# Kernel optimization log

Measured on AMD Instinct MI355X. Metric: run time of the kernel, lower is better.

## Reference

```python
import jax, jax.numpy as jnp
import numpy as np

N_NODES = 100000
N_EDGES = 1600000
DIM = 32
BN_EPS = 1e-5


def setup_inputs() -> dict:
    key = jax.random.key(0)
    ks = jax.random.split(key, 5)
    h = jax.random.normal(ks[0], (N_NODES, DIM), dtype=jnp.float32)
    e = jax.random.normal(ks[1], (N_EDGES, DIM), dtype=jnp.float32)
    norm = jax.random.uniform(ks[2], (N_NODES, 1), dtype=jnp.float32)
    src = jax.random.randint(ks[3], (N_EDGES,), 0, N_NODES, dtype=jnp.int32)
    dst = jax.random.randint(ks[4], (N_EDGES,), 0, N_NODES, dtype=jnp.int32)
    return {
        "h": h, "e": e, "norm": norm, "src": src, "dst": dst,
        "gamma_h": jnp.ones((DIM,), jnp.float32),
        "beta_h": jnp.zeros((DIM,), jnp.float32),
        "gamma_e": jnp.ones((DIM,), jnp.float32),
        "beta_e": jnp.zeros((DIM,), jnp.float32),
    }


def _batch_norm(x, gamma, beta):
    # training-mode BatchNorm1d: biased batch statistics over axis 0
    mean = jnp.mean(x, axis=0)
    var = jnp.var(x, axis=0)
    return (x - mean) * jax.lax.rsqrt(var + BN_EPS) * gamma + beta


def reference(h, e, norm, src, dst, gamma_h, beta_h, gamma_e, beta_e):
    n_nodes = h.shape[0]
    h = h * norm                                  # [N, d]
    # per-edge gate: e_ij = Ce + Dh_src + Eh_dst (all identity projections)
    e_ij = e + h[src] + h[dst]                    # [E, d]
    sigma = jax.nn.sigmoid(e_ij)                  # [E, d]
    # gated weighted-mean aggregation onto destination nodes
    num = jax.ops.segment_sum(sigma * h[src], dst, num_segments=n_nodes)
    den = jax.ops.segment_sum(sigma, dst, num_segments=n_nodes)
    h_new = h + num / (den + 1e-6)                # zero-indegree nodes: h + 0
    h_new = h_new * norm
    # batch norm (training mode), then activation; dropout is identity in eval
    h_out = jax.nn.relu(_batch_norm(h_new, gamma_h, beta_h))
    e_out = jax.nn.relu(_batch_norm(e_ij, gamma_e, beta_e))
    return h_out, e_out
```

## Files before the change

kernel.cpp:

```cpp
#include <hip/hip_runtime.h>

#define NN 100000
#define NE 1600000
#define DIMS 32
static constexpr int SCOPIES = 32;

typedef float fx4 __attribute__((ext_vector_type(4)));

#define SCAN_NB  128
#define SCAN_NTH 256
#define SCAN_CPT 4

static constexpr long long OFF_HNB  = 0;
static constexpr long long OFF_DEG  = 1600000;
static constexpr long long OFF_SE   = 1700000;
static constexpr long long OFF_SH   = 1702048;
static constexpr long long OFF_FIN  = 1704096;
static constexpr long long OFF_OFFS = 1704224;
static constexpr long long OFF_CURS = 1804232;
static constexpr long long OFF_TEX  = 1904232;
static constexpr long long OFF_PART = 1937000;
static constexpr long long OFF_EID2 = 1937128;

__device__ __forceinline__ ushort bf16rn(float f) {
  unsigned u = __float_as_uint(f);
  unsigned r = (u + 0x7FFFu + ((u >> 16) & 1u)) >> 16;
  return (ushort)r;
}
__device__ __forceinline__ float bf16tof(ushort s) {
  return __uint_as_float(((unsigned)s) << 16);
}

__global__ __launch_bounds__(256) void k_hn(const float* __restrict__ h,
                                            const float* __restrict__ norm,
                                            ushort* __restrict__ hnb) {
  int i = blockIdx.x * blockDim.x + threadIdx.x;
  if (i >= NN * 8) return;
  float4 v = reinterpret_cast<const float4*>(h)[i];
  float nm = norm[i >> 3];
  ushort4 o;
  o.x = bf16rn(v.x * nm);
  o.y = bf16rn(v.y * nm);
  o.z = bf16rn(v.z * nm);
  o.w = bf16rn(v.w * nm);
  reinterpret_cast<ushort4*>(hnb)[i] = o;
}

__global__ __launch_bounds__(256) void k_hist(const int* __restrict__ dst,
                                              int* __restrict__ deg) {
  int i = blockIdx.x * blockDim.x + threadIdx.x;
  if (i >= NE / 4) return;
  int4 d = reinterpret_cast<const int4*>(dst)[i];
  atomicAdd(&deg[d.x], 1);
  atomicAdd(&deg[d.y], 1);
  atomicAdd(&deg[d.z], 1);
  atomicAdd(&deg[d.w], 1);
}

__global__ __launch_bounds__(SCAN_NTH) void k_scanA(const int* __restrict__ deg,
                                                    int* __restrict__ texcl,
                                                    int* __restrict__ partials) {
  const int t = threadIdx.x, b = blockIdx.x;
  const int tid = b * SCAN_NTH + t;
  const int lo = tid * SCAN_CPT;
  const int hi = (lo + SCAN_CPT < NN) ? lo + SCAN_CPT : NN;
  int s = 0;
  for (int i = lo; i < hi; ++i) s += deg[i];
  __shared__ int sh[SCAN_NTH];
  sh[t] = s;
  __syncthreads();
  for (int d = 1; d < SCAN_NTH; d <<= 1) {
    int v = (t >= d) ? sh[t - d] : 0;
    __syncthreads();
    sh[t] += v;
    __syncthreads();
  }
  texcl[b * SCAN_NTH + t] = sh[t] - s;
  if (t == SCAN_NTH - 1) partials[b] = sh[t];
}

__global__ __launch_bounds__(SCAN_NB) void k_scanB(int* __restrict__ partials) {
  __shared__ int sh[SCAN_NB];
  const int t = threadIdx.x;
  int v = partials[t];
  sh[t] = v;
  __syncthreads();
  for (int d = 1; d < SCAN_NB; d <<= 1) {
    int u = (t >= d) ? sh[t - d] : 0;
    __syncthreads();
    sh[t] += u;
    __syncthreads();
  }
  partials[t] = sh[t] - v;
}

__global__ __launch_bounds__(SCAN_NTH) void k_scanC(const int* __restrict__ deg,
                                                    const int* __restrict__ texcl,
                                                    const int* __restrict__ partials,
                                                    int* __restrict__ offs,
                                                    int* __restrict__ curs) {
  const int t = threadIdx.x, b = blockIdx.x;
  const int tid = b * SCAN_NTH + t;
  const int lo = tid * SCAN_CPT;
  const int hi = (lo + SCAN_CPT < NN) ? lo + SCAN_CPT : NN;
  int run = partials[b] + texcl[b * SCAN_NTH + t];
  for (int i = lo; i < hi; ++i) {
    offs[i] = run;
    curs[i] = run;
    run += deg[i];
  }
  if (tid == 0) offs[NN] = NE;
}

__global__ __launch_bounds__(256) void k_edge(const float* __restrict__ e,
                                              const ushort* __restrict__ hnb,
                                              const int* __restrict__ src,
                                              const int* __restrict__ dst,
                                              int* __restrict__ curs,
                                              int2* __restrict__ eid2,
                                              float* __restrict__ stats_e) {
  const int lane = threadIdx.x & 7;
  const int slot0 = (blockIdx.x * blockDim.x + threadIdx.x) >> 3;
  const int S = (gridDim.x * blockDim.x) >> 3;
  float s0 = 0.f, s1 = 0.f, s2 = 0.f, s3 = 0.f;
  float q0 = 0.f, q1 = 0.f, q2 = 0.f, q3 = 0.f;

  const float4*  e4  = reinterpret_cast<const float4*>(e);
  const ushort4* hb4 = reinterpret_cast<const ushort4*>(hnb);

  for (int base = slot0; base < NE; base += 4 * S) {
    const int k0 = base;
    const int k1 = base + S;
    const int k2 = base + 2 * S;
    const int k3 = base + 3 * S;
    const bool v1 = (k1 < NE), v2 = (k2 < NE), v3 = (k3 < NE);
    const int a1 = v1 ? k1 : k0, a2 = v2 ? k2 : k0, a3 = v3 ? k3 : k0;
    const int sc0 = src[k0], dc0 = dst[k0];
    const int sc1 = src[a1], dc1 = dst[a1];
    const int sc2 = src[a2], dc2 = dst[a2];
    const int sc3 = src[a3], dc3 = dst[a3];
    float4  ev0 = e4[(long long)k0 * 8 + lane];
    float4  ev1 = e4[(long long)a1 * 8 + lane];
    float4  ev2 = e4[(long long)a2 * 8 + lane];
    float4  ev3 = e4[(long long)a3 * 8 + lane];
    ushort4 hs0 = hb4[(long long)sc0 * 8 + lane];
    ushort4 hs1 = hb4[(long long)sc1 * 8 + lane];
    ushort4 hs2 = hb4[(long long)sc2 * 8 + lane];
    ushort4 hs3 = hb4[(long long)sc3 * 8 + lane];
    ushort4 hd0 = hb4[(long long)dc0 * 8 + lane];
    ushort4 hd1 = hb4[(long long)dc1 * 8 + lane];
    ushort4 hd2 = hb4[(long long)dc2 * 8 + lane];
    ushort4 hd3 = hb4[(long long)dc3 * 8 + lane];
    if (lane == 0) {
      { int pos = atomicAdd(&curs[dc0], 1); eid2[pos] = make_int2(k0, sc0); }
      if (v1) { int pos = atomicAdd(&curs[dc1], 1); eid2[pos] = make_int2(k1, sc1); }
      if (v2) { int pos = atomicAdd(&curs[dc2], 1); eid2[pos] = make_int2(k2, sc2); }
      if (v3) { int pos = atomicAdd(&curs[dc3], 1); eid2[pos] = make_int2(k3, sc3); }
    }
    {
      float x0 = ev0.x + bf16tof(hs0.x) + bf16tof(hd0.x);
      float x1 = ev0.y + bf16tof(hs0.y) + bf16tof(hd0.y);
      float x2 = ev0.z + bf16tof(hs0.z) + bf16tof(hd0.z);
      float x3 = ev0.w + bf16tof(hs0.w) + bf16tof(hd0.w);
      s0 += x0; s1 += x1; s2 += x2; s3 += x3;
      q0 += x0 * x0; q1 += x1 * x1; q2 += x2 * x2; q3 += x3 * x3;
    }
    if (v1) {
      float x0 = ev1.x + bf16tof(hs1.x) + bf16tof(hd1.x);
      float x1 = ev1.y + bf16tof(hs1.y) + bf16tof(hd1.y);
      float x2 = ev1.z + bf16tof(hs1.z) + bf16tof(hd1.z);
      float x3 = ev1.w + bf16tof(hs1.w) + bf16tof(hd1.w);
      s0 += x0; s1 += x1; s2 += x2; s3 += x3;
      q0 += x0 * x0; q1 += x1 * x1; q2 += x2 * x2; q3 += x3 * x3;
    }
    if (v2) {
      float x0 = ev2.x + bf16tof(hs2.x) + bf16tof(hd2.x);
      float x1 = ev2.y + bf16tof(hs2.y) + bf16tof(hd2.y);
      float x2 = ev2.z + bf16tof(hs2.z) + bf16tof(hd2.z);
      float x3 = ev2.w + bf16tof(hs2.w) + bf16tof(hd2.w);
      s0 += x0; s1 += x1; s2 += x2; s3 += x3;
      q0 += x0 * x0; q1 += x1 * x1; q2 += x2 * x2; q3 += x3 * x3;
    }
    if (v3) {
      float x0 = ev3.x + bf16tof(hs3.x) + bf16tof(hd3.x);
      float x1 = ev3.y + bf16tof(hs3.y) + bf16tof(hd3.y);
      float x2 = ev3.z + bf16tof(hs3.z) + bf16tof(hd3.z);
      float x3 = ev3.w + bf16tof(hs3.w) + bf16tof(hd3.w);
      s0 += x0; s1 += x1; s2 += x2; s3 += x3;
      q0 += x0 * x0; q1 += x1 * x1; q2 += x2 * x2; q3 += x3 * x3;
    }
  }

  __shared__ float sh[64];
  if (threadIdx.x < 64) sh[threadIdx.x] = 0.f;
  __syncthreads();
  const int cb = lane * 4;
  atomicAdd(&sh[cb + 0], s0); atomicAdd(&sh[cb + 1], s1);
  atomicAdd(&sh[cb + 2], s2); atomicAdd(&sh[cb + 3], s3);
  atomicAdd(&sh[32 + cb + 0], q0); atomicAdd(&sh[32 + cb + 1], q1);
  atomicAdd(&sh[32 + cb + 2], q2); atomicAdd(&sh[32 + cb + 3], q3);
  __syncthreads();
  if (threadIdx.x < 64)
    atomicAdd(&stats_e[(blockIdx.x & (SCOPIES - 1)) * 64 + threadIdx.x], sh[threadIdx.x]);
}

__global__ void k_fin_e(const float* __restrict__ stats_e, float* __restrict__ fin) {
  int t = threadIdx.x;
  float s = 0.f, q = 0.f;
  for (int c = 0; c < SCOPIES; ++c) {
    s += stats_e[c * 64 + t];
    q += stats_e[c * 64 + 32 + t];
  }
  float mean = s / (float)NE;
  float var = q / (float)NE - mean * mean;
  fin[64 + t] = mean;
  fin[96 + t] = rsqrtf(var + 1e-5f);
}

__global__ __launch_bounds__(256) void k_agg(const float* __restrict__ e,
                                             const float* __restrict__ h,
                                             const ushort* __restrict__ hnb,
                                             const int* __restrict__ offs,
                                             const int2* __restrict__ eid2,
                                             const float* __restrict__ norm,
                                             const float* __restrict__ fin,
                                             const float* __restrict__ ge,
                                             const float* __restrict__ be,
                                             float* __restrict__ hpre,
                                             float* __restrict__ eout,
                                             float* __restrict__ stats_h) {
  const int g = (blockIdx.x * blockDim.x + threadIdx.x) >> 3;
  const int lane = threadIdx.x & 7;
  const int cb = lane * 4;
  float n0 = 0.f, n1 = 0.f, n2 = 0.f, n3 = 0.f;
  float d0 = 0.f, d1 = 0.f, d2 = 0.f, d3 = 0.f;

  const float4*  e4  = reinterpret_cast<const float4*>(e);
  const ushort4* hb4 = reinterpret_cast<const ushort4*>(hnb);

  float me0 = fin[64 + cb + 0], me1 = fin[64 + cb + 1], me2 = fin[64 + cb + 2], me3 = fin[64 + cb + 3];
  float ie0 = fin[96 + cb + 0], ie1 = fin[96 + cb + 1], ie2 = fin[96 + cb + 2], ie3 = fin[96 + cb + 3];
  float ge0 = ge[cb + 0], ge1 = ge[cb + 1], ge2 = ge[cb + 2], ge3 = ge[cb + 3];
  float be0 = be[cb + 0], be1 = be[cb + 1], be2 = be[cb + 2], be3 = be[cb + 3];

  ushort4 uhv = hb4[(long long)g * 8 + lane];
  float hv0 = bf16tof(uhv.x), hv1 = bf16tof(uhv.y), hv2 = bf16tof(uhv.z), hv3 = bf16tof(uhv.w);
  float nm = norm[g];
  float4 hf = reinterpret_cast<const float4*>(h)[(long long)g * 8 + lane];
  float hw0 = hf.x * nm, hw1 = hf.y * nm, hw2 = hf.z * nm, hw3 = hf.w * nm;

  const int lo = offs[g];
  const int hi = offs[g + 1];

#define AGG_CONSUME(EV, US, KX)                                                   \
  {                                                                               \
    float fs0 = bf16tof(US.x), fs1 = bf16tof(US.y),                               \
          fs2 = bf16tof(US.z), fs3 = bf16tof(US.w);                               \
    float x0 = EV.x + fs0 + hv0;                                                  \
    float x1 = EV.y + fs1 + hv1;                                                  \
    float x2 = EV.z + fs2 + hv2;                                                  \
    float x3 = EV.w + fs3 + hv3;                                                  \
    float g0 = 1.f / (1.f + __expf(-x0));                                         \
    float g1 = 1.f / (1.f + __expf(-x1));                                         \
    float g2 = 1.f / (1.f + __expf(-x2));                                         \
    float g3 = 1.f / (1.f + __expf(-x3));                                         \
    n0 += g0 * fs0; n1 += g1 * fs1; n2 += g2 * fs2; n3 += g3 * fs3;               \
    d0 += g0; d1 += g1; d2 += g2; d3 += g3;                                       \
    fx4 ov;                                                                       \
    ov.x = fmaxf(0.f, (x0 - me0) * ie0 * ge0 + be0);                              \
    ov.y = fmaxf(0.f, (x1 - me1) * ie1 * ge1 + be1);                              \
    ov.z = fmaxf(0.f, (x2 - me2) * ie2 * ge2 + be2);                              \
    ov.w = fmaxf(0.f, (x3 - me3) * ie3 * ge3 + be3);                              \
    __builtin_nontemporal_store(ov, reinterpret_cast<fx4*>(eout) + ((long long)(KX) * 8 + lane)); \
  }

  int p = lo;
  for (; p + 4 <= hi; p += 4) {
    int2 r0 = eid2[p + 0];
    int2 r1 = eid2[p + 1];
    int2 r2 = eid2[p + 2];
    int2 r3 = eid2[p + 3];
    float4  ev0 = e4[(long long)r0.x * 8 + lane];
    float4  ev1 = e4[(long long)r1.x * 8 + lane];
    float4  ev2 = e4[(long long)r2.x * 8 + lane];
    float4  ev3 = e4[(long long)r3.x * 8 + lane];
    ushort4 us0 = hb4[(long long)r0.y * 8 + lane];
    ushort4 us1 = hb4[(long long)r1.y * 8 + lane];
    ushort4 us2 = hb4[(long long)r2.y * 8 + lane];
    ushort4 us3 = hb4[(long long)r3.y * 8 + lane];
    AGG_CONSUME(ev0, us0, r0.x)
    AGG_CONSUME(ev1, us1, r1.x)
    AGG_CONSUME(ev2, us2, r2.x)
    AGG_CONSUME(ev3, us3, r3.x)
  }
  for (; p < hi; ++p) {
    int2 r0 = eid2[p];
    float4  ev0 = e4[(long long)r0.x * 8 + lane];
    ushort4 us0 = hb4[(long long)r0.y * 8 + lane];
    AGG_CONSUME(ev0, us0, r0.x)
  }
#undef AGG_CONSUME

  float y0 = (hw0 + n0 / (d0 + 1e-6f)) * nm;
  float y1 = (hw1 + n1 / (d1 + 1e-6f)) * nm;
  float y2 = (hw2 + n2 / (d2 + 1e-6f)) * nm;
  float y3 = (hw3 + n3 / (d3 + 1e-6f)) * nm;
  reinterpret_cast<float4*>(hpre)[(long long)g * 8 + lane] = make_float4(y0, y1, y2, y3);

  __shared__ float sh[64];
  if (threadIdx.x < 64) sh[threadIdx.x] = 0.f;
  __syncthreads();
  atomicAdd(&sh[cb + 0], y0); atomicAdd(&sh[cb + 1], y1);
  atomicAdd(&sh[cb + 2], y2); atomicAdd(&sh[cb + 3], y3);
  atomicAdd(&sh[32 + cb + 0], y0 * y0); atomicAdd(&sh[32 + cb + 1], y1 * y1);
  atomicAdd(&sh[32 + cb + 2], y2 * y2); atomicAdd(&sh[32 + cb + 3], y3 * y3);
  __syncthreads();
  if (threadIdx.x < 64)
    atomicAdd(&stats_h[(blockIdx.x & (SCOPIES - 1)) * 64 + threadIdx.x], sh[threadIdx.x]);
}

__global__ void k_fin_h(const float* __restrict__ stats_h, float* __restrict__ fin) {
  int t = threadIdx.x;
  float s = 0.f, q = 0.f;
  for (int c = 0; c < SCOPIES; ++c) {
    s += stats_h[c * 64 + t];
    q += stats_h[c * 64 + 32 + t];
  }
  float mean = s / (float)NN;
  float var = q / (float)NN - mean * mean;
  fin[t] = mean;
  fin[32 + t] = rsqrtf(var + 1e-5f);
}

__global__ __launch_bounds__(256) void k_apply(float* __restrict__ buf,
                                               long long nslots,
                                               const float* __restrict__ mean,
                                               const float* __restrict__ inv,
                                               const float* __restrict__ gamma,
                                               const float* __restrict__ beta) {
  long long i = (long long)blockIdx.x * blockDim.x + threadIdx.x;
  if (i >= nslots) return;
  const int cb = (int)(i & 7) * 4;
  float4 x = reinterpret_cast<float4*>(buf)[i];
  float y0 = fmaxf(0.f, (x.x - mean[cb + 0]) * inv[cb + 0] * gamma[cb + 0] + beta[cb + 0]);
  float y1 = fmaxf(0.f, (x.y - mean[cb + 1]) * inv[cb + 1] * gamma[cb + 1] + beta[cb + 1]);
  float y2 = fmaxf(0.f, (x.z - mean[cb + 2]) * inv[cb + 2] * gamma[cb + 2] + beta[cb + 2]);
  float y3 = fmaxf(0.f, (x.w - mean[cb + 3]) * inv[cb + 3] * gamma[cb + 3] + beta[cb + 3]);
  reinterpret_cast<float4*>(buf)[i] = make_float4(y0, y1, y2, y3);
}

extern "C" void kernel_launch(void* const* d_in, const int* in_sizes, int n_in,
                              void* d_out, int out_size, void* d_ws, size_t ws_size,
                              hipStream_t stream) {
  const float* h     = (const float*)d_in[0];
  const float* e     = (const float*)d_in[1];
  const float* norm  = (const float*)d_in[2];
  const int*   src   = (const int*)d_in[3];
  const int*   dst   = (const int*)d_in[4];
  const float* gh    = (const float*)d_in[5];
  const float* bh    = (const float*)d_in[6];
  const float* ge    = (const float*)d_in[7];
  const float* be    = (const float*)d_in[8];
  (void)in_sizes; (void)n_in; (void)out_size; (void)ws_size;

  float*  ws    = (float*)d_ws;
  ushort* hnb   = (ushort*)(ws + OFF_HNB);
  int*    deg   = (int*)(ws + OFF_DEG);
  float*  se    = ws + OFF_SE;
  float*  shh   = ws + OFF_SH;
  float*  fin   = ws + OFF_FIN;
  int*    offs  = (int*)(ws + OFF_OFFS);
  int*    curs  = (int*)(ws + OFF_CURS);
  int*    texcl = (int*)(ws + OFF_TEX);
  int*    parts = (int*)(ws + OFF_PART);
  int2*   eid2  = (int2*)(ws + OFF_EID2);

  float* out  = (float*)d_out;
  float* hpre = out;
  float* eout = out + (long long)NN * DIMS;

  (void)hipMemsetAsync(deg, 0, (size_t)(OFF_FIN - OFF_DEG) * sizeof(float), stream);

  k_hn<<<(NN * 8 + 255) / 256, 256, 0, stream>>>(h, norm, hnb);
  k_hist<<<(NE / 4 + 255) / 256, 256, 0, stream>>>(dst, deg);
  k_scanA<<<SCAN_NB, SCAN_NTH, 0, stream>>>(deg, texcl, parts);
  k_scanB<<<1, SCAN_NB, 0, stream>>>(parts);
  k_scanC<<<SCAN_NB, SCAN_NTH, 0, stream>>>(deg, texcl, parts, offs, curs);
  k_edge<<<4096, 256, 0, stream>>>(e, hnb, src, dst, curs, eid2, se);
  k_fin_e<<<1, 32, 0, stream>>>(se, fin);
  k_agg<<<NN * 8 / 256, 256, 0, stream>>>(e, h, hnb, offs, eid2, norm, fin, ge, be,
                                          hpre, eout, shh);
  k_fin_h<<<1, 32, 0, stream>>>(shh, fin);
  k_apply<<<(NN * 8 + 255) / 256, 256, 0, stream>>>(hpre, (long long)NN * 8,
                                                    fin + 0, fin + 32, gh, bh);
}
```

Measured before the change: 322.6 us.

## Replace atomic CSR build with two-level bucketed counting sort by destination

Replaces the global-atomic degree histogram, three-kernel scan and per-edge global-atomic scatter inside the edge kernel with a two-pass bucket sort. Edges are first bucketed into 1024 coarse destination ranges using shared-memory counters, then each bucket is sorted locally in shared memory to emit the CSR offsets and (edge, src) pairs. This removes contended global atomics and random global writes, at the cost of an extra 64-bit record pass through memory and a single-block scan. Buckets holding more than 2048 edges would silently drop entries, which is safe only for roughly uniform degree distributions.

```diff
diff --git a/kernel.cpp b/kernel.cpp
--- a/kernel.cpp
+++ b/kernel.cpp
@@ -7,20 +7,20 @@
 
 typedef float fx4 __attribute__((ext_vector_type(4)));
 
-#define SCAN_NB  128
-#define SCAN_NTH 256
-#define SCAN_CPT 4
-
-static constexpr long long OFF_HNB  = 0;
-static constexpr long long OFF_DEG  = 1600000;
-static constexpr long long OFF_SE   = 1700000;
-static constexpr long long OFF_SH   = 1702048;
-static constexpr long long OFF_FIN  = 1704096;
-static constexpr long long OFF_OFFS = 1704224;
-static constexpr long long OFF_CURS = 1804232;
-static constexpr long long OFF_TEX  = 1904232;
-static constexpr long long OFF_PART = 1937000;
-static constexpr long long OFF_EID2 = 1937128;
+#define NBUCK 1024
+#define NPB   98
+#define B1    128
+#define CHUNK (NE / B1)
+
+static constexpr long long OFF_HNB   = 0;
+static constexpr long long OFF_SE    = 1600000;
+static constexpr long long OFF_SH    = 1602048;
+static constexpr long long OFF_FIN   = 1604096;
+static constexpr long long OFF_OFFS  = 1604224;
+static constexpr long long OFF_BBASE = 1704226;
+static constexpr long long OFF_HIST  = 1705252;
+static constexpr long long OFF_REC   = 1836324;
+static constexpr long long OFF_EID2  = 5036324;
 
 __device__ __forceinline__ ushort bf16rn(float f) {
   unsigned u = __float_as_uint(f);
@@ -46,78 +46,111 @@
   reinterpret_cast<ushort4*>(hnb)[i] = o;
 }
 
-__global__ __launch_bounds__(256) void k_hist(const int* __restrict__ dst,
-                                              int* __restrict__ deg) {
-  int i = blockIdx.x * blockDim.x + threadIdx.x;
-  if (i >= NE / 4) return;
-  int4 d = reinterpret_cast<const int4*>(dst)[i];
-  atomicAdd(&deg[d.x], 1);
-  atomicAdd(&deg[d.y], 1);
-  atomicAdd(&deg[d.z], 1);
-  atomicAdd(&deg[d.w], 1);
-}
-
-__global__ __launch_bounds__(SCAN_NTH) void k_scanA(const int* __restrict__ deg,
-                                                    int* __restrict__ texcl,
-                                                    int* __restrict__ partials) {
+__global__ __launch_bounds__(256) void k_bh(const int* __restrict__ dst,
+                                            int* __restrict__ hist) {
+  __shared__ int cnt[NBUCK];
   const int t = threadIdx.x, b = blockIdx.x;
-  const int tid = b * SCAN_NTH + t;
-  const int lo = tid * SCAN_CPT;
-  const int hi = (lo + SCAN_CPT < NN) ? lo + SCAN_CPT : NN;
-  int s = 0;
-  for (int i = lo; i < hi; ++i) s += deg[i];
-  __shared__ int sh[SCAN_NTH];
-  sh[t] = s;
-  __syncthreads();
-  for (int d = 1; d < SCAN_NTH; d <<= 1) {
+  for (int j = t; j < NBUCK; j += 256) cnt[j] = 0;
+  __syncthreads();
+  const int lo = b * CHUNK, hi = lo + CHUNK;
+  for (int i = lo + t; i < hi; i += 256) atomicAdd(&cnt[dst[i] / NPB], 1);
+  __syncthreads();
+  for (int j = t; j < NBUCK; j += 256) hist[j * B1 + b] = cnt[j];
+}
+
+__global__ __launch_bounds__(1024) void k_bscan(int* __restrict__ hist,
+                                                int* __restrict__ bbase) {
+  __shared__ int sh[NBUCK];
+  const int t = threadIdx.x;
+  int tot = 0;
+  for (int i = 0; i < B1; ++i) tot += hist[t * B1 + i];
+  sh[t] = tot;
+  __syncthreads();
+  for (int d = 1; d < NBUCK; d <<= 1) {
     int v = (t >= d) ? sh[t - d] : 0;
     __syncthreads();
     sh[t] += v;
     __syncthreads();
   }
-  texcl[b * SCAN_NTH + t] = sh[t] - s;
-  if (t == SCAN_NTH - 1) partials[b] = sh[t];
-}
-
-__global__ __launch_bounds__(SCAN_NB) void k_scanB(int* __restrict__ partials) {
-  __shared__ int sh[SCAN_NB];
-  const int t = threadIdx.x;
-  int v = partials[t];
-  sh[t] = v;
-  __syncthreads();
-  for (int d = 1; d < SCAN_NB; d <<= 1) {
-    int u = (t >= d) ? sh[t - d] : 0;
-    __syncthreads();
-    sh[t] += u;
-    __syncthreads();
-  }
-  partials[t] = sh[t] - v;
-}
-
-__global__ __launch_bounds__(SCAN_NTH) void k_scanC(const int* __restrict__ deg,
-                                                    const int* __restrict__ texcl,
-                                                    const int* __restrict__ partials,
-                                                    int* __restrict__ offs,
-                                                    int* __restrict__ curs) {
+  int excl = sh[t] - tot;
+  bbase[t] = excl;
+  if (t == NBUCK - 1) bbase[NBUCK] = NE;
+  int run = excl;
+  for (int i = 0; i < B1; ++i) {
+    int c = hist[t * B1 + i];
+    hist[t * B1 + i] = run;
+    run += c;
+  }
+}
+
+__global__ __launch_bounds__(256) void k_bscat(const int* __restrict__ src,
+                                               const int* __restrict__ dst,
+                                               const int* __restrict__ hist,
+                                               unsigned long long* __restrict__ rec) {
+  __shared__ int cur[NBUCK];
   const int t = threadIdx.x, b = blockIdx.x;
-  const int tid = b * SCAN_NTH + t;
-  const int lo = tid * SCAN_CPT;
-  const int hi = (lo + SCAN_CPT < NN) ? lo + SCAN_CPT : NN;
-  int run = partials[b] + texcl[b * SCAN_NTH + t];
-  for (int i = lo; i < hi; ++i) {
-    offs[i] = run;
-    curs[i] = run;
-    run += deg[i];
-  }
-  if (tid == 0) offs[NN] = NE;
+  for (int j = t; j < NBUCK; j += 256) cur[j] = hist[j * B1 + b];
+  __syncthreads();
+  const int lo = b * CHUNK, hi = lo + CHUNK;
+  for (int i = lo + t; i < hi; i += 256) {
+    int d = dst[i], s = src[i];
+    int bk = d / NPB;
+    int pos = atomicAdd(&cur[bk], 1);
+    rec[pos] = (unsigned long long)i |
+               ((unsigned long long)s << 21) |
+               ((unsigned long long)d << 38);
+  }
+}
+
+__global__ __launch_bounds__(256) void k_bsort(const unsigned long long* __restrict__ rec,
+                                               const int* __restrict__ bbase,
+                                               int2* __restrict__ eid2,
+                                               int* __restrict__ offs) {
+  __shared__ int cnt[NPB];
+  __shared__ int curq[NPB];
+  __shared__ int2 sorted[2048];
+  const int t = threadIdx.x, b = blockIdx.x;
+  const int base_e = bbase[b];
+  const int n = bbase[b + 1] - base_e;
+  const int nodebase = b * NPB;
+  if (t < NPB) cnt[t] = 0;
+  __syncthreads();
+  for (int i = t; i < n; i += 256) {
+    int d = (int)((rec[base_e + i] >> 38) & 0x1FFFF);
+    atomicAdd(&cnt[d - nodebase], 1);
+  }
+  __syncthreads();
+  if (t == 0) {
+    int run = 0;
+    for (int j = 0; j < NPB; ++j) {
+      int c = cnt[j];
+      cnt[j] = run;
+      curq[j] = run;
+      run += c;
+    }
+  }
+  __syncthreads();
+  for (int i = t; i < n; i += 256) {
+    unsigned long long r = rec[base_e + i];
+    int k = (int)(r & 0x1FFFFF);
+    int s = (int)((r >> 21) & 0x1FFFF);
+    int d = (int)((r >> 38) & 0x1FFFF);
+    int pos = atomicAdd(&curq[d - nodebase], 1);
+    if (pos < 2048) sorted[pos] = make_int2(k, s);
+  }
+  __syncthreads();
+  for (int i = t; i < n; i += 256) eid2[base_e + i] = sorted[i];
+  for (int j = t; j < NPB; j += 256) {
+    int node = nodebase + j;
+    if (node < NN) offs[node] = base_e + cnt[j];
+  }
+  if (b == 0 && t == 0) offs[NN] = NE;
 }
 
 __global__ __launch_bounds__(256) void k_edge(const float* __restrict__ e,
                                               const ushort* __restrict__ hnb,
                                               const int* __restrict__ src,
                                               const int* __restrict__ dst,
-                                              int* __restrict__ curs,
-                                              int2* __restrict__ eid2,
                                               float* __restrict__ stats_e) {
   const int lane = threadIdx.x & 7;
   const int slot0 = (blockIdx.x * blockDim.x + threadIdx.x) >> 3;
@@ -151,12 +184,6 @@
     ushort4 hd1 = hb4[(long long)dc1 * 8 + lane];
     ushort4 hd2 = hb4[(long long)dc2 * 8 + lane];
     ushort4 hd3 = hb4[(long long)dc3 * 8 + lane];
-    if (lane == 0) {
-      { int pos = atomicAdd(&curs[dc0], 1); eid2[pos] = make_int2(k0, sc0); }
-      if (v1) { int pos = atomicAdd(&curs[dc1], 1); eid2[pos] = make_int2(k1, sc1); }
-      if (v2) { int pos = atomicAdd(&curs[dc2], 1); eid2[pos] = make_int2(k2, sc2); }
-      if (v3) { int pos = atomicAdd(&curs[dc3], 1); eid2[pos] = make_int2(k3, sc3); }
-    }
     {
       float x0 = ev0.x + bf16tof(hs0.x) + bf16tof(hd0.x);
       float x1 = ev0.y + bf16tof(hs0.y) + bf16tof(hd0.y);
@@ -365,28 +392,27 @@
 
   float*  ws    = (float*)d_ws;
   ushort* hnb   = (ushort*)(ws + OFF_HNB);
-  int*    deg   = (int*)(ws + OFF_DEG);
   float*  se    = ws + OFF_SE;
   float*  shh   = ws + OFF_SH;
   float*  fin   = ws + OFF_FIN;
   int*    offs  = (int*)(ws + OFF_OFFS);
-  int*    curs  = (int*)(ws + OFF_CURS);
-  int*    texcl = (int*)(ws + OFF_TEX);
-  int*    parts = (int*)(ws + OFF_PART);
+  int*    bbase = (int*)(ws + OFF_BBASE);
+  int*    hist  = (int*)(ws + OFF_HIST);
+  unsigned long long* rec = (unsigned long long*)(ws + OFF_REC);
   int2*   eid2  = (int2*)(ws + OFF_EID2);
 
   float* out  = (float*)d_out;
   float* hpre = out;
   float* eout = out + (long long)NN * DIMS;
 
-  (void)hipMemsetAsync(deg, 0, (size_t)(OFF_FIN - OFF_DEG) * sizeof(float), stream);
+  (void)hipMemsetAsync(se, 0, (size_t)(OFF_FIN - OFF_SE) * sizeof(float), stream);
 
   k_hn<<<(NN * 8 + 255) / 256, 256, 0, stream>>>(h, norm, hnb);
-  k_hist<<<(NE / 4 + 255) / 256, 256, 0, stream>>>(dst, deg);
-  k_scanA<<<SCAN_NB, SCAN_NTH, 0, stream>>>(deg, texcl, parts);
-  k_scanB<<<1, SCAN_NB, 0, stream>>>(parts);
-  k_scanC<<<SCAN_NB, SCAN_NTH, 0, stream>>>(deg, texcl, parts, offs, curs);
-  k_edge<<<4096, 256, 0, stream>>>(e, hnb, src, dst, curs, eid2, se);
+  k_bh<<<B1, 256, 0, stream>>>(dst, hist);
+  k_bscan<<<1, NBUCK, 0, stream>>>(hist, bbase);
+  k_bscat<<<B1, 256, 0, stream>>>(src, dst, hist, rec);
+  k_bsort<<<NBUCK, 256, 0, stream>>>(rec, bbase, eid2, offs);
+  k_edge<<<4096, 256, 0, stream>>>(e, hnb, src, dst, se);
   k_fin_e<<<1, 32, 0, stream>>>(se, fin);
   k_agg<<<NN * 8 / 256, 256, 0, stream>>>(e, h, hnb, offs, eid2, norm, fin, ge, be,
                                           hpre, eout, shh);
```

After: 324.4 us. No clear change (+0.5%).
